# Kernel optimization log

Hardware: AMD Instinct MI355X
Metric: run time of the kernel (lower is better)

The kernel has to match this reference:

```python
import jax, jax.numpy as jnp
import numpy as np
from jax import lax

# Surrogate spike: forward = Heaviside, backward = g / (1 + 5|x|)^2
@jax.custom_vjp
def spike_fn(x):
    return (x >= 0).astype(x.dtype)

def _spk_fwd(x):
    return spike_fn(x), x

def _spk_bwd(x, g):
    return (g / (1.0 + 5.0 * jnp.abs(x)) ** 2,)

spike_fn.defvjp(_spk_fwd, _spk_bwd)

BN_EPS = 1e-5

def _batchnorm(x, scale, bias, mean, var):
    # x: (B, C, T); eval-mode BN with running stats
    inv = scale / jnp.sqrt(var + BN_EPS)
    return x * inv[None, :, None] + (bias - mean * inv)[None, :, None]

def _conv1d(x, w, b, pad):
    y = lax.conv_general_dilated(x, w, (1,), [(pad, pad)],
                                 dimension_numbers=('NCH', 'OIH', 'NCH'))
    return y + b[None, :, None]

def setup_inputs() -> dict:
    key = jax.random.key(0)
    ks = jax.random.split(key, 12)
    B, T, EEG, GEO, TH, H, OUT = 4096, 320, 64, 18, 32, 16, 4
    inp = {
        'x_eeg': jax.random.normal(ks[0], (B, T, EEG), jnp.float32),
        'x_geo': jax.random.normal(ks[1], (B, T, GEO), jnp.float32),
        'conv1_w': jax.random.normal(ks[2], (TH, EEG, 5), jnp.float32) * 0.05,
        'conv1_b': jnp.zeros((TH,), jnp.float32),
        'bn1_s': jnp.ones((TH,), jnp.float32),
        'bn1_b': jnp.zeros((TH,), jnp.float32),
        'bn1_m': jnp.zeros((TH,), jnp.float32),
        'bn1_v': jnp.ones((TH,), jnp.float32),
        'conv2_w': jax.random.normal(ks[3], (H, TH, 3), jnp.float32) * 0.1,
        'conv2_b': jnp.zeros((H,), jnp.float32),
        'bn2_s': jnp.ones((H,), jnp.float32),
        'bn2_b': jnp.zeros((H,), jnp.float32),
        'bn2_m': jnp.zeros((H,), jnp.float32),
        'bn2_v': jnp.ones((H,), jnp.float32),
        'geo_w': jax.random.normal(ks[4], (H, GEO), jnp.float32) * 0.2,
        'geo_b': jnp.zeros((H,), jnp.float32),
        'gamma': jnp.full((H,), 0.5, jnp.float32),
        'fc1_w': jax.random.normal(ks[5], (64, 160), jnp.float32) * 0.08,
        'fc1_b': jnp.zeros((64,), jnp.float32),
        'fc2_w': jax.random.normal(ks[6], (OUT, 64), jnp.float32) * 0.12,
        'fc2_b': jnp.zeros((OUT,), jnp.float32),
    }
    return inp

def reference(x_eeg, x_geo, conv1_w, conv1_b, bn1_s, bn1_b, bn1_m, bn1_v,
              conv2_w, conv2_b, bn2_s, bn2_b, bn2_m, bn2_v,
              geo_w, geo_b, gamma, fc1_w, fc1_b, fc2_w, fc2_b):
    B, T, _ = x_eeg.shape
    theta_0, beta, tau_a, tau_m = 0.5, 1.8, 0.36, 0.8

    # EEG temporal encoder (eval mode: dropout = identity)
    h = x_eeg.transpose(0, 2, 1)  # (B, 64, T)
    h = jax.nn.relu(_batchnorm(_conv1d(h, conv1_w, conv1_b, 2), bn1_s, bn1_b, bn1_m, bn1_v))
    h = jax.nn.relu(_batchnorm(_conv1d(h, conv2_w, conv2_b, 1), bn2_s, bn2_b, bn2_m, bn2_v))
    eeg_encoded = h.transpose(0, 2, 1)  # (B, T, 16)

    geo_mod = jax.nn.sigmoid(jnp.einsum('bti,hi->bth', x_geo, geo_w) + geo_b)  # (B, T, 16)

    H = eeg_encoded.shape[-1]
    zeros = jnp.zeros((B, H), x_eeg.dtype)
    init = (zeros, zeros, zeros, zeros)  # mem_alif, eta, mem_li, prev_spk

    def step(carry, xs):
        mem_alif, eta, mem_li, prev_spk = carry
        cur_eeg, cur_geo = xs
        eta = tau_a * eta + (1.0 - tau_a) * prev_spk
        theta_t = theta_0 + beta * eta - gamma * cur_geo
        mem_alif = tau_m * mem_alif + cur_eeg
        spk = spike_fn(mem_alif - theta_t)
        mem_alif = mem_alif * (1.0 - spk)
        mem_li = 0.9 * mem_li + spk
        return (mem_alif, eta, mem_li, spk), mem_li

    xs = (eeg_encoded.transpose(1, 0, 2), geo_mod.transpose(1, 0, 2))  # (T, B, 16)
    _, pot = lax.scan(step, init, xs)  # (T, B, 16)

    pot = pot.transpose(1, 2, 0)                 # (B, 16, T)
    windows = pot.reshape(B, H, 10, 32)          # T = 320 = 10*32
    dp_feat = (windows[..., 16:].mean(-1) - windows[..., :16].mean(-1)).reshape(B, -1)  # (B, 160)

    out = jax.nn.relu(dp_feat @ fc1_w.T + fc1_b) @ fc2_w.T + fc2_b  # (B, 4)
    return out
```

## Files before the change

### kernel.cpp

```cpp
#include <hip/hip_runtime.h>
#include <math.h>

#define TB    4096
#define TSEQ  320
#define NEEG  64
#define NTH   32
#define NH    16
#define NGEO  18
#define TILE_T 64
#define NTILES 5
#define XROWS2 70
#define H1ROWS 66

typedef _Float16 f16x8 __attribute__((ext_vector_type(8)));
typedef _Float16 f16x2 __attribute__((ext_vector_type(2)));
typedef float f32x4 __attribute__((ext_vector_type(4)));
#define INV2048 4.8828125e-4f

#define OFF_W1F  0
#define OFF_W2F  10240
#define OFF_B1   11776
#define OFF_B2   11808
#define OFF_GWT  11824
#define OFF_FC1T 12112
#define OFF_FC2T 22352
#define OFF_ZP   22656
#define OFF_E    32768
#define SZ_EC    (TB*TSEQ*NH)
#define OFF_C    (OFF_E + SZ_EC)

__global__ void __launch_bounds__(256)
prep_kernel(const float* __restrict__ c1w, const float* __restrict__ c1b,
            const float* __restrict__ s1,  const float* __restrict__ bb1,
            const float* __restrict__ mm1, const float* __restrict__ vv1,
            const float* __restrict__ c2w, const float* __restrict__ c2b,
            const float* __restrict__ s2,  const float* __restrict__ bb2,
            const float* __restrict__ mm2, const float* __restrict__ vv2,
            const float* __restrict__ gw,  const float* __restrict__ fc1w,
            const float* __restrict__ fc2w, float* __restrict__ ws)
{
    const int tid = threadIdx.x;
    _Float16* w1fp = reinterpret_cast<_Float16*>(ws + OFF_W1F);
    _Float16* w2fp = reinterpret_cast<_Float16*>(ws + OFF_W2F);

    for (int d = tid; d < 10240; d += 256) {
        int j = d & 7, l = (d >> 3) & 63, nbk = d >> 9;
        int kk = nbk >> 1, nb = nbk & 1;
        int k = kk >> 1, i = (kk & 1) * 32 + ((l >> 4) * 8) + j;
        int c = nb * 16 + (l & 15);
        float inv = s1[c] / sqrtf(vv1[c] + 1e-5f);
        float wv = c1w[c * 320 + i * 5 + k] * inv;
        _Float16 hi = (_Float16)wv;
        _Float16 lo = (_Float16)((wv - (float)hi) * 2048.f);
        w1fp[((nbk * 2 + 0) * 64 + l) * 8 + j] = hi;
        w1fp[((nbk * 2 + 1) * 64 + l) * 8 + j] = lo;
    }
    for (int d = tid; d < 1536; d += 256) {
        int j = d & 7, l = (d >> 3) & 63, kk2 = d >> 9;
        int c = (l >> 4) * 8 + j;
        int o = l & 15;
        float inv = s2[o] / sqrtf(vv2[o] + 1e-5f);
        float wv = c2w[o * 96 + c * 3 + kk2] * inv;
        _Float16 hi = (_Float16)wv;
        _Float16 lo = (_Float16)((wv - (float)hi) * 2048.f);
        w2fp[((kk2 * 2 + 0) * 64 + l) * 8 + j] = hi;
        w2fp[((kk2 * 2 + 1) * 64 + l) * 8 + j] = lo;
    }
    if (tid < NTH) {
        float inv = s1[tid] / sqrtf(vv1[tid] + 1e-5f);
        ws[OFF_B1 + tid] = c1b[tid] * inv + bb1[tid] - mm1[tid] * inv;
    }
    if (tid < NH) {
        float inv = s2[tid] / sqrtf(vv2[tid] + 1e-5f);
        ws[OFF_B2 + tid] = c2b[tid] * inv + bb2[tid] - mm2[tid] * inv;
    }
    for (int d = tid; d < NGEO * NH; d += 256) {
        int i = d / NH, h = d - i * NH;
        ws[OFF_GWT + d] = gw[h * NGEO + i];
    }
    for (int d = tid; d < 160 * 64; d += 256) {
        int f = d / 64, o = d - f * 64;
        ws[OFF_FC1T + d] = fc1w[o * 160 + f];
    }
    if (tid < 256) {
        int j = tid / 4, o = tid - j * 4;
        ws[OFF_FC2T + tid] = fc2w[o * 64 + j];
    }
    if (tid < 64) ws[OFF_ZP + tid] = 0.f;
}

__global__ void __launch_bounds__(256, 2)
convm_kernel(const float* __restrict__ xeeg, const float* __restrict__ ws,
             float* __restrict__ E)
{
    __shared__ __align__(16) float xbuf[2][XROWS2 * 64];
    __shared__ __align__(16) _Float16 h1h[H1ROWS * 32];
    __shared__ __align__(16) _Float16 h1l[H1ROWS * 32];
    __shared__ float b1s[32], b2s[16];

    const int b = blockIdx.x, tid = threadIdx.x;
    const int l = tid & 63, w = tid >> 6;
    const int lrow = l & 15, lkg = l >> 4;
    const int nb = w >> 1, wsub = w & 1;

    const float* xb = xeeg + (size_t)b * TSEQ * NEEG;
    const float* zp = ws + OFF_ZP;

#define STAGE_DMA(buf, t0n) do {                                                     \
        for (int c_ = w; c_ < XROWS2; c_ += 4) {                                     \
            int tg_ = (t0n) - 3 + c_;                                                \
            const float* s_ = (tg_ >= 0 && tg_ < TSEQ)                               \
                              ? (xb + (size_t)tg_ * 64 + l) : zp;                    \
            __builtin_amdgcn_global_load_lds(                                        \
                (const __attribute__((address_space(1))) void*)s_,                   \
                (__attribute__((address_space(3))) void*)&xbuf[(buf)][c_ * 64],      \
                4, 0, 0);                                                            \
        }                                                                            \
    } while (0)

    f16x8 B1h[10], B1l[10], B2h[3], B2l[3];
    {
        const f16x8* wsrc = reinterpret_cast<const f16x8*>(ws + OFF_W1F);
        #pragma unroll
        for (int kk = 0; kk < 10; ++kk) {
            B1h[kk] = wsrc[((kk * 2 + nb) * 2 + 0) * 64 + l];
            B1l[kk] = wsrc[((kk * 2 + nb) * 2 + 1) * 64 + l];
        }
        const f16x8* wsrc2 = reinterpret_cast<const f16x8*>(ws + OFF_W2F);
        #pragma unroll
        for (int kk = 0; kk < 3; ++kk) {
            B2h[kk] = wsrc2[(kk * 2 + 0) * 64 + l];
            B2l[kk] = wsrc2[(kk * 2 + 1) * 64 + l];
        }
    }
    if (tid < 32) b1s[tid] = ws[OFF_B1 + tid];
    if (tid < 16) b2s[tid] = ws[OFF_B2 + tid];

    STAGE_DMA(0, 0);
    __syncthreads();

    for (int jt = 0; jt < NTILES; ++jt) {
        const int t0 = jt * TILE_T;
        const int cur = jt & 1;
        _Float16* xh = reinterpret_cast<_Float16*>(&xbuf[cur][0]);
        _Float16* xl = xh + XROWS2 * 64;

        float2 xr2[9];
        #pragma unroll
        for (int q = 0; q < 9; ++q) {
            int p = tid + q * 256;
            if (p < 2240) {
                int xr = p >> 5, ip = (p & 31) * 2;
                xr2[q] = *reinterpret_cast<const float2*>(&xbuf[cur][xr * 64 + ip]);
            }
        }
        __syncthreads();

        #pragma unroll
        for (int q = 0; q < 9; ++q) {
            int p = tid + q * 256;
            if (p < 2240) {
                int xr = p >> 5, ip = (p & 31) * 2;
                float f0 = xr2[q].x, f1 = xr2[q].y;
                _Float16 h0 = (_Float16)f0, h1v = (_Float16)f1;
                f16x2 vh = {h0, h1v};
                f16x2 vl = {(_Float16)((f0 - (float)h0) * 2048.f),
                            (_Float16)((f1 - (float)h1v) * 2048.f)};
                int idx = xr * 64 + (((ip >> 3) ^ (xr & 7)) << 3) + (ip & 7);
                *reinterpret_cast<f16x2*>(&xh[idx]) = vh;
                *reinterpret_cast<f16x2*>(&xl[idx]) = vl;
            }
        }
        __syncthreads();

        if (jt + 1 < NTILES) STAGE_DMA(cur ^ 1, (jt + 1) * TILE_T);
        __builtin_amdgcn_s_setprio(1);
        {
            const float bia = b1s[nb * 16 + lrow];
            #pragma unroll
            for (int pi = 0; pi < 3; ++pi) {
                if (pi == 2 && ((jt & 1) != wsub)) break;
                const int mb = (pi < 2) ? (wsub + pi * 2) : 4;
                const int mbase = mb * 16;
                int s = mbase + lrow; if (s > 65) s = 65;
                f32x4 aH = {0.f, 0.f, 0.f, 0.f};
                f32x4 aM = aH, aL = aH;
                #pragma unroll
                for (int kk = 0; kk < 10; ++kk) {
                    const int xr = s + (kk >> 1);
                    const int gx = (kk & 1) * 4 + lkg;
                    const int off = xr * 64 + ((gx ^ (xr & 7)) << 3);
                    f16x8 Ah = *reinterpret_cast<const f16x8*>(&xh[off]);
                    f16x8 Al = *reinterpret_cast<const f16x8*>(&xl[off]);
                    aH = __builtin_amdgcn_mfma_f32_16x16x32_f16(Ah, B1h[kk], aH, 0, 0, 0);
                    aM = __builtin_amdgcn_mfma_f32_16x16x32_f16(Ah, B1l[kk], aM, 0, 0, 0);
                    aL = __builtin_amdgcn_mfma_f32_16x16x32_f16(Al, B1h[kk], aL, 0, 0, 0);
                }
                #pragma unroll
                for (int r = 0; r < 4; ++r) {
                    int so = mbase + lkg * 4 + r;
                    if (so < 66) {
                        int tg = t0 - 1 + so;
                        bool v = (tg >= 0 && tg < TSEQ);
                        float val = v ? fmaxf(fmaf(aM[r] + aL[r], INV2048, aH[r]) + bia, 0.f) : 0.f;
                        int key = (so >> 1) & 3;
                        int g = (nb * 2 + (lrow >> 3)) ^ key;
                        int idx = so * 32 + (g << 3) + (lrow & 7);
                        _Float16 hh = (_Float16)val;
                        h1h[idx] = hh;
                        h1l[idx] = (_Float16)((val - (float)hh) * 2048.f);
                    }
                }
            }
        }
        __builtin_amdgcn_s_setprio(0);
        __syncthreads();

        {
            const int ub = w * 16;
            f32x4 aH = {0.f, 0.f, 0.f, 0.f};
            f32x4 aM = aH, aL = aH;
            __builtin_amdgcn_s_setprio(1);
            #pragma unroll
            for (int kk = 0; kk < 3; ++kk) {
                int srow = ub + lrow + kk;
                int off = srow * 32 + ((lkg ^ ((srow >> 1) & 3)) << 3);
                f16x8 Ah = *reinterpret_cast<const f16x8*>(&h1h[off]);
                f16x8 Al = *reinterpret_cast<const f16x8*>(&h1l[off]);
                aH = __builtin_amdgcn_mfma_f32_16x16x32_f16(Ah, B2h[kk], aH, 0, 0, 0);
                aM = __builtin_amdgcn_mfma_f32_16x16x32_f16(Ah, B2l[kk], aM, 0, 0, 0);
                aL = __builtin_amdgcn_mfma_f32_16x16x32_f16(Al, B2h[kk], aL, 0, 0, 0);
            }
            __builtin_amdgcn_s_setprio(0);
            const float bia = b2s[lrow];
            float4 ev;
            float* evp = reinterpret_cast<float*>(&ev);
            #pragma unroll
            for (int r = 0; r < 4; ++r)
                evp[r] = fmaxf(fmaf(aM[r] + aL[r], INV2048, aH[r]) + bia, 0.f);
            const int t4o = ((t0 + ub) >> 2) + lkg;
            float* ep = E + (((size_t)t4o * TB + b) * 16 + lrow) * 4;
            *reinterpret_cast<float4*>(ep) = ev;
        }
    }
#undef STAGE_DMA
}

__global__ void __launch_bounds__(256)
geo_kernel(const float* __restrict__ xgeo, const float* __restrict__ ws,
           const float* __restrict__ geo_b, const float* __restrict__ gamma,
           float* __restrict__ C)
{
    __shared__ float xgs[16][72];
    __shared__ float gws_l[NGEO * NH];
    __shared__ float gb_l[16], gam_l[16];

    const int tid = threadIdx.x;
    const int b0 = blockIdx.x * 16;
    const int t4 = blockIdx.y;

    for (int p = tid; p < NGEO * NH; p += 256) gws_l[p] = ws[OFF_GWT + p];
    if (tid < 16) { gb_l[tid] = geo_b[tid]; gam_l[tid] = gamma[tid]; }
    for (int p = tid; p < 16 * 72; p += 256) {
        int bb = p / 72, r = p - bb * 72;
        xgs[bb][r] = xgeo[(size_t)(b0 + bb) * (TSEQ * NGEO) + (size_t)t4 * 72 + r];
    }
    __syncthreads();

    const int h = tid & 15, bl = tid >> 4;
    float4 cv;
    float* cvp = reinterpret_cast<float*>(&cv);
    #pragma unroll
    for (int tt = 0; tt < 4; ++tt) {
        float z = gb_l[h];
        const float* xr = &xgs[bl][tt * 18];
        #pragma unroll
        for (int ii = 0; ii < NGEO; ++ii)
            z = fmaf(xr[ii], gws_l[ii * 16 + h], z);
        cvp[tt] = gam_l[h] * (1.f / (1.f + expf(-z)));
    }
    float* cp = C + (((size_t)t4 * TB + (b0 + bl)) * 16 + h) * 4;
    *reinterpret_cast<float4*>(cp) = cv;
}

__global__ void __launch_bounds__(256)
scanfc_kernel(const float* __restrict__ E, const float* __restrict__ C,
              const float* __restrict__ ws, const float* __restrict__ fc1_b,
              const float* __restrict__ fc2_b, float* __restrict__ out)
{
    __shared__ float dp_lds[16][160];
    __shared__ float mid[16][64];

    const int tid = threadIdx.x;
    const int h = tid & 15, bl = tid >> 4;
    const int b0 = blockIdx.x * 16;
    const int b = b0 + bl;

    const float4* e4 = reinterpret_cast<const float4*>(E);
    const float4* c4 = reinterpret_cast<const float4*>(C);
    const size_t slab = (size_t)TB * 16;
    const size_t idx = (size_t)b * 16 + h;

    float eta = 0.f, memv = 0.f, li = 0.f, ps = 0.f, accF = 0.f, accS = 0.f;
    float4 ev = e4[idx], cv = c4[idx];
    for (int t4 = 0; t4 < 80; ++t4) {
        float4 en, cn;
        if (t4 < 79) {
            en = e4[(size_t)(t4 + 1) * slab + idx];
            cn = c4[(size_t)(t4 + 1) * slab + idx];
        }
        const float* evp = reinterpret_cast<const float*>(&ev);
        const float* cvp = reinterpret_cast<const float*>(&cv);
        #pragma unroll
        for (int tt = 0; tt < 4; ++tt) {
            float e = evp[tt], c = cvp[tt];
            eta = 0.36f * eta + 0.64f * ps;
            float theta = 0.5f + 1.8f * eta - c;
            memv = 0.8f * memv + e;
            float spk = (memv - theta >= 0.f) ? 1.f : 0.f;
            memv *= (1.f - spk);
            li = 0.9f * li + spk;
            ps = spk;
            int t = t4 * 4 + tt;
            if (((t >> 4) & 1) == 0) accF += li; else accS += li;
        }
        if ((t4 & 7) == 7) {
            dp_lds[bl][h * 10 + (t4 >> 3)] = (accS - accF) * 0.0625f;
            accF = 0.f; accS = 0.f;
        }
        ev = en; cv = cn;
    }
    __syncthreads();

    {
        const float* __restrict__ fc1t = ws + OFF_FC1T;
        #pragma unroll
        for (int k = 0; k < 4; ++k) {
            int id = tid + k * 256;
            int bb = id >> 6, o = id & 63;
            float z = fc1_b[o];
            for (int f = 0; f < 160; ++f)
                z = fmaf(dp_lds[bb][f], fc1t[f * 64 + o], z);
            mid[bb][o] = fmaxf(z, 0.f);
        }
    }
    __syncthreads();
    if (tid < 64) {
        const float* __restrict__ fc2t = ws + OFF_FC2T;
        int bb = tid >> 2, oo = tid & 3;
        float z = fc2_b[oo];
        #pragma unroll
        for (int jj = 0; jj < 64; ++jj)
            z = fmaf(mid[bb][jj], fc2t[jj * 4 + oo], z);
        out[(size_t)(b0 + bb) * 4 + oo] = z;
    }
}

extern "C" void kernel_launch(void* const* d_in, const int* in_sizes, int n_in,
                              void* d_out, int out_size, void* d_ws, size_t ws_size,
                              hipStream_t stream)
{
    const float* xeeg = (const float*)d_in[0];
    const float* xgeo = (const float*)d_in[1];
    const float* c1w  = (const float*)d_in[2];
    const float* c1b  = (const float*)d_in[3];
    const float* s1   = (const float*)d_in[4];
    const float* bb1  = (const float*)d_in[5];
    const float* mm1  = (const float*)d_in[6];
    const float* vv1  = (const float*)d_in[7];
    const float* c2w  = (const float*)d_in[8];
    const float* c2b  = (const float*)d_in[9];
    const float* s2   = (const float*)d_in[10];
    const float* bb2  = (const float*)d_in[11];
    const float* mm2  = (const float*)d_in[12];
    const float* vv2  = (const float*)d_in[13];
    const float* gw   = (const float*)d_in[14];
    const float* gb   = (const float*)d_in[15];
    const float* gam  = (const float*)d_in[16];
    const float* fc1w = (const float*)d_in[17];
    const float* fc1b = (const float*)d_in[18];
    const float* fc2w = (const float*)d_in[19];
    const float* fc2b = (const float*)d_in[20];
    float* ws   = (float*)d_ws;
    float* outp = (float*)d_out;

    hipLaunchKernelGGL(prep_kernel, dim3(1), dim3(256), 0, stream,
                       c1w, c1b, s1, bb1, mm1, vv1, c2w, c2b, s2, bb2, mm2, vv2,
                       gw, fc1w, fc2w, ws);

    float* E = ws + OFF_E;
    float* C = ws + OFF_C;
    hipLaunchKernelGGL(geo_kernel, dim3(TB / 16, TSEQ / 4), dim3(256), 0, stream,
                       xgeo, ws, gb, gam, C);
    hipLaunchKernelGGL(convm_kernel, dim3(TB), dim3(256), 0, stream,
                       xeeg, ws, E);
    hipLaunchKernelGGL(scanfc_kernel, dim3(TB / 16), dim3(256), 0, stream,
                       E, C, ws, fc1b, fc2b, outp);
}
```

Measured before the change: 323.8 us.

## Merge geo kernel into conv launch and deepen scan prefetch pipeline

The sigmoid geo-modulation kernel becomes extra blocks appended to the conv kernel's grid, so both run in one launch and can overlap on the device. The scan kernel's one-step-ahead prefetch is replaced by double-buffered groups of four float4 loads, keeping more memory requests in flight during the serial recurrence. The trade-offs are higher register pressure in the scan, plus extra LDS declared in the conv kernel, which could hurt its occupancy under the launch bound of 2.

```diff
diff --git a/kernel.cpp b/kernel.cpp
--- a/kernel.cpp
+++ b/kernel.cpp
@@ -11,6 +11,7 @@
 #define NTILES 5
 #define XROWS2 70
 #define H1ROWS 66
+#define NGEOBLK ((TB/16)*80)
 
 typedef _Float16 f16x8 __attribute__((ext_vector_type(8)));
 typedef _Float16 f16x2 __attribute__((ext_vector_type(2)));
@@ -90,15 +91,52 @@
 }
 
 __global__ void __launch_bounds__(256, 2)
-convm_kernel(const float* __restrict__ xeeg, const float* __restrict__ ws,
-             float* __restrict__ E)
+convm_kernel(const float* __restrict__ xeeg, const float* __restrict__ xgeo,
+             const float* __restrict__ ws,   const float* __restrict__ geo_b,
+             const float* __restrict__ gamma,
+             float* __restrict__ E, float* __restrict__ C)
 {
     __shared__ __align__(16) float xbuf[2][XROWS2 * 64];
     __shared__ __align__(16) _Float16 h1h[H1ROWS * 32];
     __shared__ __align__(16) _Float16 h1l[H1ROWS * 32];
     __shared__ float b1s[32], b2s[16];
-
-    const int b = blockIdx.x, tid = threadIdx.x;
+    __shared__ float xgs[16][72];
+    __shared__ float gws_l[NGEO * NH];
+    __shared__ float gb_l[16], gam_l[16];
+
+    const int tid = threadIdx.x;
+
+    if (blockIdx.x >= TB) {
+        const int g = blockIdx.x - TB;
+        const int b0 = (g & 255) * 16;
+        const int t4 = g >> 8;
+
+        for (int p = tid; p < NGEO * NH; p += 256) gws_l[p] = ws[OFF_GWT + p];
+        if (tid < 16) { gb_l[tid] = geo_b[tid]; gam_l[tid] = gamma[tid]; }
+        for (int p = tid; p < 16 * 72; p += 256) {
+            int bb = p / 72, r = p - bb * 72;
+            xgs[bb][r] = xgeo[(size_t)(b0 + bb) * (TSEQ * NGEO) + (size_t)t4 * 72 + r];
+        }
+        __syncthreads();
+
+        const int h = tid & 15, bl = tid >> 4;
+        float4 cv;
+        float* cvp = reinterpret_cast<float*>(&cv);
+        #pragma unroll
+        for (int tt = 0; tt < 4; ++tt) {
+            float z = gb_l[h];
+            const float* xr = &xgs[bl][tt * 18];
+            #pragma unroll
+            for (int ii = 0; ii < NGEO; ++ii)
+                z = fmaf(xr[ii], gws_l[ii * 16 + h], z);
+            cvp[tt] = gam_l[h] * (1.f / (1.f + expf(-z)));
+        }
+        float* cp = C + (((size_t)t4 * TB + (b0 + bl)) * 16 + h) * 4;
+        *reinterpret_cast<float4*>(cp) = cv;
+        return;
+    }
+
+    const int b = blockIdx.x;
     const int l = tid & 63, w = tid >> 6;
     const int lrow = l & 15, lkg = l >> 4;
     const int nb = w >> 1, wsub = w & 1;
@@ -247,43 +285,6 @@
 }
 
 __global__ void __launch_bounds__(256)
-geo_kernel(const float* __restrict__ xgeo, const float* __restrict__ ws,
-           const float* __restrict__ geo_b, const float* __restrict__ gamma,
-           float* __restrict__ C)
-{
-    __shared__ float xgs[16][72];
-    __shared__ float gws_l[NGEO * NH];
-    __shared__ float gb_l[16], gam_l[16];
-
-    const int tid = threadIdx.x;
-    const int b0 = blockIdx.x * 16;
-    const int t4 = blockIdx.y;
-
-    for (int p = tid; p < NGEO * NH; p += 256) gws_l[p] = ws[OFF_GWT + p];
-    if (tid < 16) { gb_l[tid] = geo_b[tid]; gam_l[tid] = gamma[tid]; }
-    for (int p = tid; p < 16 * 72; p += 256) {
-        int bb = p / 72, r = p - bb * 72;
-        xgs[bb][r] = xgeo[(size_t)(b0 + bb) * (TSEQ * NGEO) + (size_t)t4 * 72 + r];
-    }
-    __syncthreads();
-
-    const int h = tid & 15, bl = tid >> 4;
-    float4 cv;
-    float* cvp = reinterpret_cast<float*>(&cv);
-    #pragma unroll
-    for (int tt = 0; tt < 4; ++tt) {
-        float z = gb_l[h];
-        const float* xr = &xgs[bl][tt * 18];
-        #pragma unroll
-        for (int ii = 0; ii < NGEO; ++ii)
-            z = fmaf(xr[ii], gws_l[ii * 16 + h], z);
-        cvp[tt] = gam_l[h] * (1.f / (1.f + expf(-z)));
-    }
-    float* cp = C + (((size_t)t4 * TB + (b0 + bl)) * 16 + h) * 4;
-    *reinterpret_cast<float4*>(cp) = cv;
-}
-
-__global__ void __launch_bounds__(256)
 scanfc_kernel(const float* __restrict__ E, const float* __restrict__ C,
               const float* __restrict__ ws, const float* __restrict__ fc1_b,
               const float* __restrict__ fc2_b, float* __restrict__ out)
@@ -302,34 +303,55 @@
     const size_t idx = (size_t)b * 16 + h;
 
     float eta = 0.f, memv = 0.f, li = 0.f, ps = 0.f, accF = 0.f, accS = 0.f;
-    float4 ev = e4[idx], cv = c4[idx];
-    for (int t4 = 0; t4 < 80; ++t4) {
-        float4 en, cn;
-        if (t4 < 79) {
-            en = e4[(size_t)(t4 + 1) * slab + idx];
-            cn = c4[(size_t)(t4 + 1) * slab + idx];
-        }
-        const float* evp = reinterpret_cast<const float*>(&ev);
-        const float* cvp = reinterpret_cast<const float*>(&cv);
-        #pragma unroll
-        for (int tt = 0; tt < 4; ++tt) {
-            float e = evp[tt], c = cvp[tt];
-            eta = 0.36f * eta + 0.64f * ps;
-            float theta = 0.5f + 1.8f * eta - c;
-            memv = 0.8f * memv + e;
-            float spk = (memv - theta >= 0.f) ? 1.f : 0.f;
-            memv *= (1.f - spk);
-            li = 0.9f * li + spk;
-            ps = spk;
-            int t = t4 * 4 + tt;
-            if (((t >> 4) & 1) == 0) accF += li; else accS += li;
-        }
-        if ((t4 & 7) == 7) {
-            dp_lds[bl][h * 10 + (t4 >> 3)] = (accS - accF) * 0.0625f;
-            accF = 0.f; accS = 0.f;
-        }
-        ev = en; cv = cn;
-    }
+
+    float4 eA[4], cA[4], eB[4], cB[4];
+
+#define LOADQ(EB, CB, lq) do {                                                   \
+        if ((lq) < 20) {                                                         \
+            _Pragma("unroll")                                                    \
+            for (int j = 0; j < 4; ++j) {                                        \
+                EB[j] = e4[(size_t)((lq) * 4 + j) * slab + idx];                 \
+                CB[j] = c4[(size_t)((lq) * 4 + j) * slab + idx];                 \
+            }                                                                    \
+        }                                                                        \
+    } while (0)
+
+#define PROCQ(EB, CB, q) do {                                                    \
+        _Pragma("unroll")                                                        \
+        for (int j = 0; j < 4; ++j) {                                            \
+            const int t4_ = (q) * 4 + j;                                         \
+            const float* evp = reinterpret_cast<const float*>(&EB[j]);           \
+            const float* cvp = reinterpret_cast<const float*>(&CB[j]);           \
+            _Pragma("unroll")                                                    \
+            for (int tt = 0; tt < 4; ++tt) {                                     \
+                float e = evp[tt], c = cvp[tt];                                  \
+                eta = 0.36f * eta + 0.64f * ps;                                  \
+                float theta = 0.5f + 1.8f * eta - c;                             \
+                memv = 0.8f * memv + e;                                          \
+                float spk = (memv - theta >= 0.f) ? 1.f : 0.f;                   \
+                memv *= (1.f - spk);                                             \
+                li = 0.9f * li + spk;                                            \
+                ps = spk;                                                        \
+                int t = t4_ * 4 + tt;                                            \
+                if (((t >> 4) & 1) == 0) accF += li; else accS += li;            \
+            }                                                                    \
+            if ((t4_ & 7) == 7) {                                                \
+                dp_lds[bl][h * 10 + (t4_ >> 3)] = (accS - accF) * 0.0625f;       \
+                accF = 0.f; accS = 0.f;                                          \
+            }                                                                    \
+        }                                                                        \
+    } while (0)
+
+    LOADQ(eA, cA, 0);
+    for (int qp = 0; qp < 10; ++qp) {
+        const int q0 = qp * 2, q1 = qp * 2 + 1;
+        LOADQ(eB, cB, q1);
+        PROCQ(eA, cA, q0);
+        LOADQ(eA, cA, q1 + 1);
+        PROCQ(eB, cB, q1);
+    }
+#undef LOADQ
+#undef PROCQ
     __syncthreads();
 
     {
@@ -390,10 +412,8 @@
 
     float* E = ws + OFF_E;
     float* C = ws + OFF_C;
-    hipLaunchKernelGGL(geo_kernel, dim3(TB / 16, TSEQ / 4), dim3(256), 0, stream,
-                       xgeo, ws, gb, gam, C);
-    hipLaunchKernelGGL(convm_kernel, dim3(TB), dim3(256), 0, stream,
-                       xeeg, ws, E);
+    hipLaunchKernelGGL(convm_kernel, dim3(TB + NGEOBLK), dim3(256), 0, stream,
+                       xeeg, xgeo, ws, gb, gam, E, C);
     hipLaunchKernelGGL(scanfc_kernel, dim3(TB / 16), dim3(256), 0, stream,
                        E, C, ws, fc1b, fc2b, outp);
 }
```

Result: slower. 407.6 us (+25.9%).
